# Performance work log

Measured on AMD Instinct MI355X. Metric: run time of the kernel, lower is better.

## Reference

```python
import jax, jax.numpy as jnp
import numpy as np
import math

HIDDEN = 2048
N_HEADS = 16
KV_CHANNELS = 128
HEAD_DIM = 2 * KV_CHANNELS  # per-head dim used by this module (256)
SEQ = 2048
BATCH = 2
W_SCALE = 0.02


def setup_inputs() -> dict:
    key = jax.random.key(0)
    k1, k2, k3 = jax.random.split(key, 3)
    hidden_states = jax.random.normal(k1, (SEQ, BATCH, 2 * HIDDEN), dtype=jnp.float32)
    attention_mask = jnp.zeros((SEQ, SEQ), dtype=bool)  # accepted but unused, as in source
    w_qkv = jax.random.normal(k2, (6 * HIDDEN, 2 * HIDDEN), dtype=jnp.float32) * W_SCALE
    w_proj = jax.random.normal(k3, (HIDDEN, 2 * HIDDEN), dtype=jnp.float32) * W_SCALE
    return {"hidden_states": hidden_states, "attention_mask": attention_mask,
            "w_qkv": w_qkv, "w_proj": w_proj}


def _attention_forward(hidden_states, w_qkv, w_proj):
    s, b, _ = hidden_states.shape
    # QKV projection: [s, b, 6*HIDDEN]
    qkv = jnp.einsum('sbe,fe->sbf', hidden_states, w_qkv)
    # reshape to [s, b, groups, (h/g + 2) * head_dim]; here groups == heads, h/g == 1
    qkv = qkv.reshape(s, b, N_HEADS, 3 * HEAD_DIM)
    q, k, v = jnp.split(qkv, [HEAD_DIM, 2 * HEAD_DIM], axis=3)  # each [s,b,h,256]
    # scaling = 1.0 / rsqrt(kv_channels) == sqrt(kv_channels) (faithful to source)
    scale = math.sqrt(KV_CHANNELS)
    scores = jnp.einsum('sbhe,tbhe->bhst', q, k) * scale  # [b,h,s,s]
    causal = jnp.triu(jnp.ones((s, s), dtype=bool), k=1)
    scores = jnp.where(causal[None, None, :, :], -jnp.inf, scores)
    probs = jax.nn.softmax(scores.astype(jnp.float32), axis=-1).astype(q.dtype)
    y = jnp.einsum('bhst,tbhe->sbhe', probs, v)  # [s,b,h,256]
    y = y.reshape(s, b, N_HEADS * HEAD_DIM)  # [s,b,2*HIDDEN]
    out = jnp.einsum('sbf,of->sbo', y, w_proj)  # [s,b,HIDDEN]
    return out


def reference(hidden_states, attention_mask, w_qkv, w_proj):
    # attention_mask is unused by the original forward on this code path
    return _attention_forward(hidden_states, w_qkv, w_proj)
```

## Files before the change

### kernel.cpp

```cpp
#include <hip/hip_runtime.h>
#include <stdint.h>

typedef unsigned short u16;
typedef __attribute__((ext_vector_type(4))) float f32x4;
typedef __attribute__((ext_vector_type(8))) __bf16 bf16x8;

typedef __attribute__((address_space(1))) void as1_void;
typedef __attribute__((address_space(3))) void as3_void;

#define SCALE_Q 11.313708498984761f

static_assert(sizeof(bf16x8) == 16, "bf16x8 must be 16B");

__device__ __forceinline__ u16 f2bf(float x) {
  union { float f; unsigned u; } v; v.f = x;
  return (u16)((v.u + 0x7FFFu + ((v.u >> 16) & 1u)) >> 16);
}
__device__ __forceinline__ float bf2f(u16 h) {
  union { unsigned u; float f; } v; v.u = ((unsigned)h) << 16;
  return v.f;
}
__device__ __forceinline__ f32x4 mfma16(bf16x8 a, bf16x8 b, f32x4 c) {
  return __builtin_amdgcn_mfma_f32_16x16x32_bf16(a, b, c, 0, 0, 0);
}
__device__ __forceinline__ void gload_lds16(const void* g, void* lds) {
  __builtin_amdgcn_global_load_lds((as1_void*)g, (as3_void*)lds, 16, 0, 0);
}

__global__ void k_convert(const float* __restrict__ X, u16* __restrict__ Xh,
                          u16* __restrict__ Xl) {
  long idx = ((long)blockIdx.x * 256 + threadIdx.x) * 8;
  float4 a = *(const float4*)(X + idx);
  float4 b = *(const float4*)(X + idx + 4);
  float xs[8] = {a.x, a.y, a.z, a.w, b.x, b.y, b.z, b.w};
  union { u16 s[8]; uint4 v; } hu, lu;
#pragma unroll
  for (int i = 0; i < 8; ++i) {
    u16 h = f2bf(xs[i]);
    hu.s[i] = h;
    lu.s[i] = f2bf(xs[i] - bf2f(h));
  }
  *(uint4*)(Xh + idx) = hu.v;
  *(uint4*)(Xl + idx) = lu.v;
}

__launch_bounds__(512, 2)
__global__ void k_qkv2(const u16* __restrict__ Xh, const u16* __restrict__ Xl,
                       const u16* __restrict__ Wh, const u16* __restrict__ Wl,
                       u16* __restrict__ Qh, u16* __restrict__ Ql,
                       u16* __restrict__ Kh, u16* __restrict__ Kl,
                       u16* __restrict__ Vv) {
  const int bid = blockIdx.x;
  const int swz = (bid & 7) * 96 + (bid >> 3);
  const int nt = swz % 48, mt = swz / 48;
  const int n0 = nt * 256, m0 = mt * 256;
  const int seg = (n0 % 768) / 256;
  const bool qk = (seg < 2);
  const int hblk = n0 / 768;

  __shared__ u16 S[2][2][256 * 64];

  const int tid = threadIdx.x;
  const int lane = tid & 63, w = tid >> 6;
  const int wm = w >> 2, wn = w & 3;
  const int l15 = lane & 15, l4 = lane >> 4;

  const bool stB = (w >= 4);
  const int r_in = lane >> 3;
  const int c_in = lane & 7;
  const u16* g_hi = stB ? Wh : Xh;
  const u16* g_lo = stB ? Wl : Xl;
  const int gr0 = (stB ? n0 : m0);

  const int sh = (l4 ^ (l15 & 7)) * 8;
  const int sl = ((l4 ^ 4) ^ (l15 & 7)) * 8;

  const f32x4 zero4 = {0.f, 0.f, 0.f, 0.f};
  f32x4 acc[8][4];
#pragma unroll
  for (int i = 0; i < 8; i++)
#pragma unroll
    for (int j = 0; j < 4; j++) acc[i][j] = zero4;

  if (qk) {
    auto stage = [&](int buf, int k0) {
#pragma unroll
      for (int q8 = 0; q8 < 8; ++q8) {
        const int qi = (w & 3) * 8 + q8;
        const int row = qi * 8 + r_in;
        const int cs = c_in ^ (row & 7);
        const u16* src = (cs < 4) ? g_hi : g_lo;
        const int col = k0 + (cs & 3) * 8;
        gload_lds16(src + (size_t)(gr0 + row) * 4096 + col, &S[buf][stB ? 1 : 0][qi * 512]);
      }
    };
    stage(0, 0);
    __syncthreads();
    for (int t = 0; t < 128; ++t) {
      const int cur = t & 1;
      if (t + 1 < 128) stage(cur ^ 1, (t + 1) * 32);
      const u16* sAc = &S[cur][0][0];
      const u16* sBc = &S[cur][1][0];
      bf16x8 ah[8], al[8];
#pragma unroll
      for (int i = 0; i < 8; i++) {
        const int rb = (wm * 128 + i * 16 + l15) * 64;
        ah[i] = *(const bf16x8*)&sAc[rb + sh];
        al[i] = *(const bf16x8*)&sAc[rb + sl];
      }
      __builtin_amdgcn_s_setprio(1);
#pragma unroll
      for (int j = 0; j < 4; j++) {
        const int rb = (wn * 64 + j * 16 + l15) * 64;
        bf16x8 bh = *(const bf16x8*)&sBc[rb + sh];
        bf16x8 bl = *(const bf16x8*)&sBc[rb + sl];
#pragma unroll
        for (int i = 0; i < 8; i++) {
          acc[i][j] = mfma16(ah[i], bh, acc[i][j]);
          acc[i][j] = mfma16(ah[i], bl, acc[i][j]);
          acc[i][j] = mfma16(al[i], bh, acc[i][j]);
        }
      }
      __builtin_amdgcn_s_setprio(0);
      __syncthreads();
    }
  } else {
    auto stage = [&](int buf, int k0) {
#pragma unroll
      for (int q8 = 0; q8 < 8; ++q8) {
        const int qi = (w & 3) * 8 + q8;
        const int row = qi * 8 + r_in;
        const int cs = c_in ^ (row & 7);
        gload_lds16(g_hi + (size_t)(gr0 + row) * 4096 + k0 + cs * 8, &S[buf][stB ? 1 : 0][qi * 512]);
      }
    };
    stage(0, 0);
    __syncthreads();
    for (int t = 0; t < 64; ++t) {
      const int cur = t & 1;
      if (t + 1 < 64) stage(cur ^ 1, (t + 1) * 64);
      const u16* sAc = &S[cur][0][0];
      const u16* sBc = &S[cur][1][0];
      __builtin_amdgcn_s_setprio(1);
#pragma unroll
      for (int kc = 0; kc < 2; kc++) {
        const int so = ((kc * 4 + l4) ^ (l15 & 7)) * 8;
        bf16x8 av[8];
#pragma unroll
        for (int i = 0; i < 8; i++)
          av[i] = *(const bf16x8*)&sAc[(wm * 128 + i * 16 + l15) * 64 + so];
#pragma unroll
        for (int j = 0; j < 4; j++) {
          bf16x8 bv = *(const bf16x8*)&sBc[(wn * 64 + j * 16 + l15) * 64 + so];
#pragma unroll
          for (int i = 0; i < 8; i++) acc[i][j] = mfma16(av[i], bv, acc[i][j]);
        }
      }
      __builtin_amdgcn_s_setprio(0);
      __syncthreads();
    }
  }

#pragma unroll
  for (int i = 0; i < 8; i++)
#pragma unroll
    for (int j = 0; j < 4; j++)
#pragma unroll
      for (int jj = 0; jj < 4; jj++) {
        const int mrow = m0 + wm * 128 + i * 16 + l4 * 4 + jj;
        const int ecol = wn * 64 + j * 16 + l15;
        const int srow = mrow >> 1, b = mrow & 1;
        const size_t o = ((size_t)(b * 16 + hblk) * 2048 + srow) * 256 + ecol;
        float v = acc[i][j][jj];
        if (seg == 0) {
          v *= SCALE_Q;
          u16 hb = f2bf(v);
          Qh[o] = hb;
          Ql[o] = f2bf(v - bf2f(hb));
        } else if (seg == 1) {
          u16 hb = f2bf(v);
          Kh[o] = hb;
          Kl[o] = f2bf(v - bf2f(hb));
        } else {
          Vv[o] = f2bf(v);
        }
      }
}

__global__ void k_transpose(const u16* __restrict__ Vv, u16* __restrict__ Vt) {
  const int bidx = blockIdx.x;
  const int et = bidx & 3;
  const int st = (bidx >> 2) & 31;
  const int bh = bidx >> 7;
  const int s0 = st * 64, e0 = et * 64;
  __shared__ u16 T[64][72];
  const int t = threadIdx.x;
  const int r = t >> 2, c = t & 3;
  const u16* src = Vv + (size_t)bh * 524288 + (size_t)(s0 + r) * 256 + e0 + c * 16;
  uint4 a = *(const uint4*)src;
  uint4 b = *(const uint4*)(src + 8);
  *(uint4*)&T[r][c * 16] = a;
  *(uint4*)&T[r][c * 16 + 8] = b;
  __syncthreads();
  union { u16 s[16]; uint4 v[2]; } pk;
#pragma unroll
  for (int i = 0; i < 16; i++) pk.s[i] = T[c * 16 + i][r];
  u16* dst = Vt + (size_t)bh * 524288 + (size_t)(e0 + r) * 2048 + s0 + c * 16;
  *(uint4*)dst = pk.v[0];
  *(uint4*)(dst + 8) = pk.v[1];
}

__launch_bounds__(256, 1)
__global__ void k_attn(const u16* __restrict__ Qh, const u16* __restrict__ Ql,
                       const u16* __restrict__ Kh, const u16* __restrict__ Kl,
                       const u16* __restrict__ Vt, u16* __restrict__ Y) {
  const int pairIdx = blockIdx.x & 15;
  const int bh = blockIdx.x >> 4;
  const int b = bh >> 4, h = bh & 15;
  const int tid = threadIdx.x, lane = tid & 63, w = tid >> 6;
  const int l15 = lane & 15, l4 = lane >> 4;

  __shared__ u16 SKh[2][32 * 256];
  __shared__ u16 SKl[2][32 * 256];
  __shared__ u16 SV[2][256 * 32];
  __shared__ u16 sP[64 * 40];

  const u16* Qhb = Qh + (size_t)bh * 524288;
  const u16* Qlb = Ql + (size_t)bh * 524288;
  const u16* Khb = Kh + (size_t)bh * 524288;
  const u16* Klb = Kl + (size_t)bh * 524288;
  const u16* Vtb = Vt + (size_t)bh * 524288;

  const int kr_in = lane >> 5;
  const int ks_in = lane & 31;
  const int vr_in = lane >> 2;
  const int vs_in = lane & 3;

  const f32x4 zero4 = {0.f, 0.f, 0.f, 0.f};

  for (int rep = 0; rep < 2; ++rep) {
    const int tile = rep ? (31 - pairIdx) : pairIdx;
    const int q0 = tile * 64;
    bf16x8 qfh[8], qfl[8];
    {
      const int qrow = q0 + 16 * w + l15;
      const u16* ph = Qhb + (size_t)qrow * 256 + l4 * 8;
      const u16* pl = Qlb + (size_t)qrow * 256 + l4 * 8;
#pragma unroll
      for (int kc = 0; kc < 8; kc++) {
        qfh[kc] = *(const bf16x8*)(ph + kc * 32);
        qfl[kc] = *(const bf16x8*)(pl + kc * 32);
      }
    }
    f32x4 acc[16];
#pragma unroll
    for (int ef = 0; ef < 16; ef++) acc[ef] = zero4;
    float m_run[4], l_run[4];
#pragma unroll
    for (int jj = 0; jj < 4; jj++) { m_run[jj] = -1e30f; l_run[jj] = 0.f; }

    const int nsteps = 2 * tile + 2;

    auto stage = [&](int buf, int k0) {
#pragma unroll
      for (int q4 = 0; q4 < 4; ++q4) {
        const int qi = w * 4 + q4;
        {
          const int row = qi * 2 + kr_in;
          const int cs = ks_in ^ (row & 7);
          const size_t src = (size_t)(k0 + row) * 256 + cs * 8;
          gload_lds16(Khb + src, &SKh[buf][qi * 512]);
          gload_lds16(Klb + src, &SKl[buf][qi * 512]);
        }
        {
          const int row = qi * 16 + vr_in;
          const int cs = vs_in ^ (row & 3);
          gload_lds16(Vtb + (size_t)row * 2048 + k0 + cs * 8, &SV[buf][qi * 512]);
        }
      }
    };

    stage(0, 0);
    __syncthreads();

    for (int st2 = 0; st2 < nsteps; ++st2) {
      const int k0 = st2 * 32;
      const int cur = st2 & 1;
      if (st2 + 1 < nsteps) stage(cur ^ 1, k0 + 32);
      f32x4 shh[2], shl[2], slh[2];
#pragma unroll
      for (int cf = 0; cf < 2; cf++) { shh[cf] = zero4; shl[cf] = zero4; slh[cf] = zero4; }
      __builtin_amdgcn_s_setprio(1);
#pragma unroll
      for (int kc = 0; kc < 8; kc++) {
#pragma unroll
        for (int cf = 0; cf < 2; cf++) {
          const int row = cf * 16 + l15;
          const int eo = row * 256 + (((kc * 4 + l4) ^ (row & 7)) << 3);
          bf16x8 kbh = *(const bf16x8*)&SKh[cur][eo];
          bf16x8 kbl = *(const bf16x8*)&SKl[cur][eo];
          shh[cf] = mfma16(qfh[kc], kbh, shh[cf]);
          shl[cf] = mfma16(qfh[kc], kbl, shl[cf]);
          slh[cf] = mfma16(qfl[kc], kbh, slh[cf]);
        }
      }
      __builtin_amdgcn_s_setprio(0);
      float rr[4];
#pragma unroll
      for (int jj = 0; jj < 4; jj++) {
        const int prow = 16 * w + l4 * 4 + jj;
        const int qrow = q0 + prow;
        float s0v = shh[0][jj] + shl[0][jj] + slh[0][jj];
        float s1v = shh[1][jj] + shl[1][jj] + slh[1][jj];
        if (k0 + l15 > qrow) s0v = -1e30f;
        if (k0 + 16 + l15 > qrow) s1v = -1e30f;
        float mx = fmaxf(s0v, s1v);
#pragma unroll
        for (int off = 1; off < 16; off <<= 1) mx = fmaxf(mx, __shfl_xor(mx, off, 64));
        const float mnew = fmaxf(m_run[jj], mx);
        const float r = __expf(m_run[jj] - mnew);
        const float p0 = __expf(s0v - mnew);
        const float p1 = __expf(s1v - mnew);
        float rs = p0 + p1;
#pragma unroll
        for (int off = 1; off < 16; off <<= 1) rs += __shfl_xor(rs, off, 64);
        l_run[jj] = l_run[jj] * r + rs;
        m_run[jj] = mnew;
        rr[jj] = r;
        sP[prow * 40 + l15] = f2bf(p0);
        sP[prow * 40 + 16 + l15] = f2bf(p1);
      }
#pragma unroll
      for (int ef = 0; ef < 16; ef++)
#pragma unroll
        for (int jj = 0; jj < 4; jj++) acc[ef][jj] *= rr[jj];
      bf16x8 pa = *(const bf16x8*)&sP[(16 * w + l15) * 40 + l4 * 8];
      __builtin_amdgcn_s_setprio(1);
#pragma unroll
      for (int ef = 0; ef < 16; ef++) {
        const int row = ef * 16 + l15;
        bf16x8 vb = *(const bf16x8*)&SV[cur][row * 32 + ((l4 ^ (row & 3)) << 3)];
        acc[ef] = mfma16(pa, vb, acc[ef]);
      }
      __builtin_amdgcn_s_setprio(0);
      __syncthreads();
    }
    float li[4];
#pragma unroll
    for (int jj = 0; jj < 4; jj++) li[jj] = 1.0f / l_run[jj];
#pragma unroll
    for (int ef = 0; ef < 16; ef++)
#pragma unroll
      for (int jj = 0; jj < 4; jj++) {
        const int qrow = q0 + 16 * w + l4 * 4 + jj;
        const int mrow = qrow * 2 + b;
        const int col = h * 256 + ef * 16 + l15;
        Y[(size_t)mrow * 4096 + col] = f2bf(acc[ef][jj] * li[jj]);
      }
  }
}

__launch_bounds__(256, 2)
__global__ void k_proj(const u16* __restrict__ Yb, const u16* __restrict__ Wph,
                       float* __restrict__ Out) {
  const int n0 = blockIdx.x * 128;
  const int m0 = blockIdx.y * 128;
  __shared__ u16 sA[128 * 64];
  __shared__ u16 sB[128 * 64];
  const int tid = threadIdx.x;
  const int lane = tid & 63, w = tid >> 6;
  const int wr = w >> 1, wc = w & 1;
  const int l15 = lane & 15, l4 = lane >> 4;
  const f32x4 zero4 = {0.f, 0.f, 0.f, 0.f};
  f32x4 acc[4][4];
#pragma unroll
  for (int i = 0; i < 4; i++)
#pragma unroll
    for (int j = 0; j < 4; j++) acc[i][j] = zero4;

  for (int k0 = 0; k0 < 4096; k0 += 64) {
#pragma unroll
    for (int ii = 0; ii < 4; ++ii) {
      const int inst = w * 4 + ii;
      const int o = inst * 1024 + lane * 16;
      const int mr = o >> 7, c = (o & 127) >> 4;
      const int cs = c ^ (mr & 7);
      gload_lds16(Yb + (size_t)(m0 + mr) * 4096 + k0 + cs * 8, (char*)sA + inst * 1024);
      gload_lds16(Wph + (size_t)(n0 + mr) * 4096 + k0 + cs * 8, (char*)sB + inst * 1024);
    }
    __syncthreads();
#pragma unroll
    for (int kc = 0; kc < 2; ++kc) {
      bf16x8 af[4], bff[4];
#pragma unroll
      for (int i = 0; i < 4; i++) {
        const int mr = wr * 64 + i * 16 + l15;
        const int ch = (kc * 4 + l4) ^ (mr & 7);
        af[i] = *(const bf16x8*)&sA[mr * 64 + ch * 8];
      }
#pragma unroll
      for (int j = 0; j < 4; j++) {
        const int nr = wc * 64 + j * 16 + l15;
        const int ch = (kc * 4 + l4) ^ (nr & 7);
        bff[j] = *(const bf16x8*)&sB[nr * 64 + ch * 8];
      }
#pragma unroll
      for (int i = 0; i < 4; i++)
#pragma unroll
        for (int j = 0; j < 4; j++) acc[i][j] = mfma16(af[i], bff[j], acc[i][j]);
    }
    __syncthreads();
  }
#pragma unroll
  for (int i = 0; i < 4; i++)
#pragma unroll
    for (int j = 0; j < 4; j++)
#pragma unroll
      for (int jj = 0; jj < 4; jj++) {
        const int mrow = m0 + wr * 64 + i * 16 + l4 * 4 + jj;
        const int ncol = n0 + wc * 64 + j * 16 + l15;
        Out[(size_t)mrow * 2048 + ncol] = acc[i][j][jj];
      }
}

extern "C" void kernel_launch(void* const* d_in, const int* in_sizes, int n_in,
                              void* d_out, int out_size, void* d_ws, size_t ws_size,
                              hipStream_t stream) {
  (void)in_sizes; (void)n_in; (void)out_size; (void)ws_size;
  const float* X = (const float*)d_in[0];
  const float* Wq = (const float*)d_in[2];
  const float* Wp = (const float*)d_in[3];
  float* Out = (float*)d_out;
  char* ws = (char*)d_ws;
  const size_t MB = 1ull << 20;
  u16* Xh = (u16*)(ws + 0 * 32 * MB);
  u16* Xl = (u16*)(ws + 1 * 32 * MB);
  u16* Qh = (u16*)(ws + 2 * 32 * MB);
  u16* Ql = (u16*)(ws + 3 * 32 * MB);
  u16* Kh = (u16*)(ws + 4 * 32 * MB);
  u16* Kl = (u16*)(ws + 5 * 32 * MB);
  u16* Vv = (u16*)(ws + 6 * 32 * MB);
  u16* Wh = (u16*)(ws + 224 * MB);
  u16* Wl = (u16*)(ws + 320 * MB);
  u16* Vt = Wh;
  u16* Y = Wl;
  u16* Wph = Kh;
  u16* Wpl = Kl;

  k_convert<<<8192, 256, 0, stream>>>(X, Xh, Xl);
  k_convert<<<24576, 256, 0, stream>>>(Wq, Wh, Wl);
  k_qkv2<<<768, 512, 0, stream>>>(Xh, Xl, Wh, Wl, Qh, Ql, Kh, Kl, Vv);
  k_transpose<<<4096, 256, 0, stream>>>(Vv, Vt);
  k_attn<<<512, 256, 0, stream>>>(Qh, Ql, Kh, Kl, Vt, Y);
  k_convert<<<4096, 256, 0, stream>>>(Wp, Wph, Wpl);
  k_proj<<<dim3(16, 32), 256, 0, stream>>>(Y, Wph, Out);
}
```

Measured before the change: 1.510 ms.

## Enlarge attention and projection tiles to 512-thread blocks with double-buffered GEMM

Measured after the change: 1.349 ms, median of 2. 1.12x faster.

```diff
diff --git a/kernel.cpp b/kernel.cpp
--- a/kernel.cpp
+++ b/kernel.cpp
@@ -210,12 +210,14 @@
   *(uint4*)(dst + 8) = pk.v[1];
 }
 
-__launch_bounds__(256, 1)
+__launch_bounds__(512, 1)
 __global__ void k_attn(const u16* __restrict__ Qh, const u16* __restrict__ Ql,
                        const u16* __restrict__ Kh, const u16* __restrict__ Kl,
                        const u16* __restrict__ Vt, u16* __restrict__ Y) {
-  const int pairIdx = blockIdx.x & 15;
-  const int bh = blockIdx.x >> 4;
+  const int bid = blockIdx.x;
+  const int swz = (bid & 7) * 32 + (bid >> 3);
+  const int bh = swz >> 3;
+  const int pairIdx = swz & 7;
   const int b = bh >> 4, h = bh & 15;
   const int tid = threadIdx.x, lane = tid & 63, w = tid >> 6;
   const int l15 = lane & 15, l4 = lane >> 4;
@@ -223,7 +225,7 @@
   __shared__ u16 SKh[2][32 * 256];
   __shared__ u16 SKl[2][32 * 256];
   __shared__ u16 SV[2][256 * 32];
-  __shared__ u16 sP[64 * 40];
+  __shared__ u16 sP[128 * 40];
 
   const u16* Qhb = Qh + (size_t)bh * 524288;
   const u16* Qlb = Ql + (size_t)bh * 524288;
@@ -239,8 +241,8 @@
   const f32x4 zero4 = {0.f, 0.f, 0.f, 0.f};
 
   for (int rep = 0; rep < 2; ++rep) {
-    const int tile = rep ? (31 - pairIdx) : pairIdx;
-    const int q0 = tile * 64;
+    const int tile = rep ? (15 - pairIdx) : pairIdx;
+    const int q0 = tile * 128;
     bf16x8 qfh[8], qfl[8];
     {
       const int qrow = q0 + 16 * w + l15;
@@ -259,12 +261,12 @@
 #pragma unroll
     for (int jj = 0; jj < 4; jj++) { m_run[jj] = -1e30f; l_run[jj] = 0.f; }
 
-    const int nsteps = 2 * tile + 2;
+    const int nsteps = 4 * tile + 4;
 
     auto stage = [&](int buf, int k0) {
 #pragma unroll
-      for (int q4 = 0; q4 < 4; ++q4) {
-        const int qi = w * 4 + q4;
+      for (int q2 = 0; q2 < 2; ++q2) {
+        const int qi = w * 2 + q2;
         {
           const int row = qi * 2 + kr_in;
           const int cs = ks_in ^ (row & 7);
@@ -357,68 +359,88 @@
         const int col = h * 256 + ef * 16 + l15;
         Y[(size_t)mrow * 4096 + col] = f2bf(acc[ef][jj] * li[jj]);
       }
+    __syncthreads();
   }
 }
 
-__launch_bounds__(256, 2)
+__launch_bounds__(512, 1)
 __global__ void k_proj(const u16* __restrict__ Yb, const u16* __restrict__ Wph,
                        float* __restrict__ Out) {
-  const int n0 = blockIdx.x * 128;
-  const int m0 = blockIdx.y * 128;
-  __shared__ u16 sA[128 * 64];
-  __shared__ u16 sB[128 * 64];
+  const int bid = blockIdx.x;
+  const int swz = (bid & 7) * 32 + (bid >> 3);
+  const int nt = swz % 16, mt = swz / 16;
+  const int n0 = nt * 128, m0 = mt * 256;
+
+  __shared__ u16 SA[2][256 * 64];
+  __shared__ u16 SB[2][128 * 64];
+
   const int tid = threadIdx.x;
   const int lane = tid & 63, w = tid >> 6;
-  const int wr = w >> 1, wc = w & 1;
+  const int wm = w >> 2, wn = w & 3;
   const int l15 = lane & 15, l4 = lane >> 4;
+
+  const bool stB = (w >= 4);
+  const int r_in = lane >> 3;
+  const int c_in = lane & 7;
+
   const f32x4 zero4 = {0.f, 0.f, 0.f, 0.f};
-  f32x4 acc[4][4];
-#pragma unroll
-  for (int i = 0; i < 4; i++)
-#pragma unroll
-    for (int j = 0; j < 4; j++) acc[i][j] = zero4;
-
-  for (int k0 = 0; k0 < 4096; k0 += 64) {
-#pragma unroll
-    for (int ii = 0; ii < 4; ++ii) {
-      const int inst = w * 4 + ii;
-      const int o = inst * 1024 + lane * 16;
-      const int mr = o >> 7, c = (o & 127) >> 4;
-      const int cs = c ^ (mr & 7);
-      gload_lds16(Yb + (size_t)(m0 + mr) * 4096 + k0 + cs * 8, (char*)sA + inst * 1024);
-      gload_lds16(Wph + (size_t)(n0 + mr) * 4096 + k0 + cs * 8, (char*)sB + inst * 1024);
-    }
-    __syncthreads();
-#pragma unroll
-    for (int kc = 0; kc < 2; ++kc) {
-      bf16x8 af[4], bff[4];
-#pragma unroll
-      for (int i = 0; i < 4; i++) {
-        const int mr = wr * 64 + i * 16 + l15;
-        const int ch = (kc * 4 + l4) ^ (mr & 7);
-        af[i] = *(const bf16x8*)&sA[mr * 64 + ch * 8];
-      }
-#pragma unroll
-      for (int j = 0; j < 4; j++) {
-        const int nr = wc * 64 + j * 16 + l15;
-        const int ch = (kc * 4 + l4) ^ (nr & 7);
-        bff[j] = *(const bf16x8*)&sB[nr * 64 + ch * 8];
-      }
-#pragma unroll
-      for (int i = 0; i < 4; i++)
-#pragma unroll
-        for (int j = 0; j < 4; j++) acc[i][j] = mfma16(af[i], bff[j], acc[i][j]);
-    }
+  f32x4 acc[8][2];
+#pragma unroll
+  for (int i = 0; i < 8; i++)
+#pragma unroll
+    for (int j = 0; j < 2; j++) acc[i][j] = zero4;
+
+  auto stage = [&](int buf, int k0) {
+    if (!stB) {
+#pragma unroll
+      for (int q8 = 0; q8 < 8; ++q8) {
+        const int qi = w * 8 + q8;
+        const int row = qi * 8 + r_in;
+        const int cs = c_in ^ (row & 7);
+        gload_lds16(Yb + (size_t)(m0 + row) * 4096 + k0 + cs * 8, &SA[buf][qi * 512]);
+      }
+    } else {
+#pragma unroll
+      for (int q4 = 0; q4 < 4; ++q4) {
+        const int qi = (w - 4) * 4 + q4;
+        const int row = qi * 8 + r_in;
+        const int cs = c_in ^ (row & 7);
+        gload_lds16(Wph + (size_t)(n0 + row) * 4096 + k0 + cs * 8, &SB[buf][qi * 512]);
+      }
+    }
+  };
+
+  stage(0, 0);
+  __syncthreads();
+  for (int t = 0; t < 64; ++t) {
+    const int cur = t & 1;
+    if (t + 1 < 64) stage(cur ^ 1, (t + 1) * 64);
+    __builtin_amdgcn_s_setprio(1);
+#pragma unroll
+    for (int kc = 0; kc < 2; kc++) {
+      const int so = ((kc * 4 + l4) ^ (l15 & 7)) * 8;
+      bf16x8 av[8];
+#pragma unroll
+      for (int i = 0; i < 8; i++)
+        av[i] = *(const bf16x8*)&SA[cur][(wm * 128 + i * 16 + l15) * 64 + so];
+#pragma unroll
+      for (int j = 0; j < 2; j++) {
+        bf16x8 bv = *(const bf16x8*)&SB[cur][(wn * 32 + j * 16 + l15) * 64 + so];
+#pragma unroll
+        for (int i = 0; i < 8; i++) acc[i][j] = mfma16(av[i], bv, acc[i][j]);
+      }
+    }
+    __builtin_amdgcn_s_setprio(0);
     __syncthreads();
   }
 #pragma unroll
-  for (int i = 0; i < 4; i++)
-#pragma unroll
-    for (int j = 0; j < 4; j++)
+  for (int i = 0; i < 8; i++)
+#pragma unroll
+    for (int j = 0; j < 2; j++)
 #pragma unroll
       for (int jj = 0; jj < 4; jj++) {
-        const int mrow = m0 + wr * 64 + i * 16 + l4 * 4 + jj;
-        const int ncol = n0 + wc * 64 + j * 16 + l15;
+        const int mrow = m0 + wm * 128 + i * 16 + l4 * 4 + jj;
+        const int ncol = n0 + wn * 32 + j * 16 + l15;
         Out[(size_t)mrow * 2048 + ncol] = acc[i][j][jj];
       }
 }
@@ -451,7 +473,7 @@
   k_convert<<<24576, 256, 0, stream>>>(Wq, Wh, Wl);
   k_qkv2<<<768, 512, 0, stream>>>(Xh, Xl, Wh, Wl, Qh, Ql, Kh, Kl, Vv);
   k_transpose<<<4096, 256, 0, stream>>>(Vv, Vt);
-  k_attn<<<512, 256, 0, stream>>>(Qh, Ql, Kh, Kl, Vt, Y);
+  k_attn<<<256, 512, 0, stream>>>(Qh, Ql, Kh, Kl, Vt, Y);
   k_convert<<<4096, 256, 0, stream>>>(Wp, Wph, Wpl);
-  k_proj<<<dim3(16, 32), 256, 0, stream>>>(Y, Wph, Out);
-}
+  k_proj<<<256, 512, 0, stream>>>(Y, Wph, Out);
+}
```
